# Kernel optimization log

Measured on AMD Instinct MI355X. Metric: run time of the kernel, lower is better.

Reference implementation:

```python
import jax, jax.numpy as jnp
import numpy as np

INV_SCALE_SQ = 0.25  # module __init__ arg
N_SITES = 65536
SITE_DIM = 5  # (x, y, r, g, b)
H, W = 2048, 2048


def setup_inputs() -> dict:
    key = jax.random.key(0)
    k1, k2, k3, k4 = jax.random.split(key, 4)
    # site positions uniform over the image, colors uniform in [0,1]
    pos = jax.random.uniform(k1, (N_SITES, 2), dtype=jnp.float32) * jnp.array([W, H], jnp.float32)
    col = jax.random.uniform(k2, (N_SITES, 3), dtype=jnp.float32)
    sites = jnp.concatenate([pos, col], axis=-1)  # [N,5]
    cand0 = jax.random.randint(k3, (H, W), 0, N_SITES, dtype=jnp.int32)
    cand1 = jax.random.randint(k4, (H, W), 0, N_SITES, dtype=jnp.int32)
    return {"sites": sites, "cand0": cand0, "cand1": cand1, "width": W, "height": H}


def reference(sites, cand0, cand1, width, height):
    # per-pixel soft (anti-aliased) Voronoi rasterization of colored sites
    xs = jnp.arange(width, dtype=jnp.float32) + 0.5
    ys = jnp.arange(height, dtype=jnp.float32) + 0.5
    px = jnp.stack(jnp.meshgrid(xs, ys, indexing="xy"), axis=-1)  # [H,W,2] pixel centers
    s0 = sites[cand0]  # [H,W,5] gather candidate 0
    s1 = sites[cand1]  # [H,W,5] gather candidate 1
    d0 = jnp.sum((px - s0[..., :2]) ** 2, axis=-1)  # squared dist to site0
    d1 = jnp.sum((px - s1[..., :2]) ** 2, axis=-1)
    w = jax.nn.sigmoid((d1 - d0) * INV_SCALE_SQ)[..., None]  # weight toward closer site0
    out = w * s0[..., 2:] + (1.0 - w) * s1[..., 2:]  # [H,W,3]
    return out
```

## Files before the change

### kernel.cpp

```cpp
#include <hip/hip_runtime.h>
#include <hip/hip_fp16.h>


#define IMG_W 2048
#define IMG_H 2048
#define N_PIX (IMG_W * IMG_H)
#define N_SITES 65536
#define INV_SCALE_SQ 0.25f

typedef int   vint4   __attribute__((ext_vector_type(4)));
typedef float vfloat4 __attribute__((ext_vector_type(4)));

__global__ __launch_bounds__(256) void repack_sites(
    const float* __restrict__ sites, vfloat4* __restrict__ packed)
{
    const int i = blockIdx.x * blockDim.x + threadIdx.x;
    const float* s = sites + (size_t)i * 5;
    const __half2 rg = __floats2half2_rn(s[2], s[3]);
    const __half2 b0 = __floats2half2_rn(s[4], 0.0f);
    vfloat4 v;
    v.x = s[0];
    v.y = s[1];
    v.z = __uint_as_float(*reinterpret_cast<const unsigned int*>(&rg));
    v.w = __uint_as_float(*reinterpret_cast<const unsigned int*>(&b0));
    packed[i] = v;
}

__device__ __forceinline__ float3 unpack_rgb(const vfloat4& rec) {
    const unsigned int zu = __float_as_uint(rec.z);
    const unsigned int wu = __float_as_uint(rec.w);
    const __half2 rg = *reinterpret_cast<const __half2*>(&zu);
    const __half2 b0 = *reinterpret_cast<const __half2*>(&wu);
    const float2 rgf = __half22float2(rg);
    return make_float3(rgf.x, rgf.y, __half2float(b0.x));
}

__global__ __launch_bounds__(256) void voronoi_soft_kernel(
    const vfloat4* __restrict__ packed,
    const int*     __restrict__ cand0,
    const int*     __restrict__ cand1,
    float*         __restrict__ out)
{
    const int tid = blockIdx.x * blockDim.x + threadIdx.x;
    const int pix = tid * 4;

    const vint4 c0 = __builtin_nontemporal_load(reinterpret_cast<const vint4*>(cand0 + pix));
    const vint4 c1 = __builtin_nontemporal_load(reinterpret_cast<const vint4*>(cand1 + pix));
    const int idx0[4] = {c0.x, c0.y, c0.z, c0.w};
    const int idx1[4] = {c1.x, c1.y, c1.z, c1.w};

    vfloat4 r0[4], r1[4];
#pragma unroll
    for (int i = 0; i < 4; ++i) r0[i] = packed[idx0[i]];
#pragma unroll
    for (int i = 0; i < 4; ++i) r1[i] = packed[idx1[i]];

    const float py = (float)(pix >> 11) + 0.5f;
    const float px_base = (float)(pix & (IMG_W - 1)) + 0.5f;

    float res[12];
#pragma unroll
    for (int i = 0; i < 4; ++i) {
        const float px = px_base + (float)i;
        const float dx0 = px - r0[i].x, dy0 = py - r0[i].y;
        const float dx1 = px - r1[i].x, dy1 = py - r1[i].y;
        const float d0 = dx0 * dx0 + dy0 * dy0;
        const float d1 = dx1 * dx1 + dy1 * dy1;

        const float t = (d1 - d0) * INV_SCALE_SQ;
        const float w = 1.0f / (1.0f + __expf(-t));
        const float wc = 1.0f - w;

        const float3 cA = unpack_rgb(r0[i]);
        const float3 cB = unpack_rgb(r1[i]);
        res[i * 3 + 0] = w * cA.x + wc * cB.x;
        res[i * 3 + 1] = w * cA.y + wc * cB.y;
        res[i * 3 + 2] = w * cA.z + wc * cB.z;
    }

    vfloat4* o = reinterpret_cast<vfloat4*>(out + (size_t)pix * 3);
    vfloat4 o0 = {res[0], res[1], res[2], res[3]};
    vfloat4 o1 = {res[4], res[5], res[6], res[7]};
    vfloat4 o2 = {res[8], res[9], res[10], res[11]};
    o[0] = o0;
    o[1] = o1;
    o[2] = o2;
}

__global__ __launch_bounds__(256) void voronoi_soft_fallback(
    const float* __restrict__ sites,
    const int*   __restrict__ cand0,
    const int*   __restrict__ cand1,
    float*       __restrict__ out)
{
    const int tid = blockIdx.x * blockDim.x + threadIdx.x;
    const int pix = tid * 4;
    const int4 c0 = *reinterpret_cast<const int4*>(cand0 + pix);
    const int4 c1 = *reinterpret_cast<const int4*>(cand1 + pix);
    const int idx0[4] = {c0.x, c0.y, c0.z, c0.w};
    const int idx1[4] = {c1.x, c1.y, c1.z, c1.w};
    const float py = (float)(pix >> 11) + 0.5f;
    const float px_base = (float)(pix & (IMG_W - 1)) + 0.5f;
    float res[12];
#pragma unroll
    for (int i = 0; i < 4; ++i) {
        const float px = px_base + (float)i;
        const float* s0 = sites + (size_t)idx0[i] * 5;
        const float* s1 = sites + (size_t)idx1[i] * 5;
        const float dx0 = px - s0[0], dy0 = py - s0[1];
        const float dx1 = px - s1[0], dy1 = py - s1[1];
        const float d0 = dx0 * dx0 + dy0 * dy0;
        const float d1 = dx1 * dx1 + dy1 * dy1;
        const float w = 1.0f / (1.0f + __expf(-(d1 - d0) * INV_SCALE_SQ));
        const float wc = 1.0f - w;
        res[i * 3 + 0] = w * s0[2] + wc * s1[2];
        res[i * 3 + 1] = w * s0[3] + wc * s1[3];
        res[i * 3 + 2] = w * s0[4] + wc * s1[4];
    }
    float4* o = reinterpret_cast<float4*>(out + (size_t)pix * 3);
    o[0] = make_float4(res[0], res[1], res[2], res[3]);
    o[1] = make_float4(res[4], res[5], res[6], res[7]);
    o[2] = make_float4(res[8], res[9], res[10], res[11]);
}

extern "C" void kernel_launch(void* const* d_in, const int* in_sizes, int n_in,
                              void* d_out, int out_size, void* d_ws, size_t ws_size,
                              hipStream_t stream) {
    const float* sites = (const float*)d_in[0];
    const int*   cand0 = (const int*)d_in[1];
    const int*   cand1 = (const int*)d_in[2];
    float* out = (float*)d_out;

    const int threads = 256;
    const int blocks = N_PIX / (4 * threads);

    const size_t packed_bytes = (size_t)N_SITES * sizeof(vfloat4);
    if (ws_size >= packed_bytes) {
        vfloat4* packed = (vfloat4*)d_ws;
        repack_sites<<<N_SITES / 256, 256, 0, stream>>>(sites, packed);
        voronoi_soft_kernel<<<blocks, threads, 0, stream>>>(packed, cand0, cand1, out);
    } else {
        voronoi_soft_fallback<<<blocks, threads, 0, stream>>>(sites, cand0, cand1, out);
    }
}
```

Measured before the change: 136.2 us.

## Process eight pixels per thread with inline-asm gathers and staged waitcnt

Each thread now handles eight pixels instead of four, issuing all sixteen site gathers up front through inline global_load_dwordx4 assembly with the sc0 cache bit. A partial s_waitcnt lets the first four pixels be shaded while the second batch of loads is still in flight. The goal is more memory-level parallelism per thread to hide gather latency. In exchange, register pressure rises, the grid has half as many threads, and hand-written waitcnt code bypasses compiler scheduling and depends on it counting outstanding loads correctly.

```diff
diff --git a/kernel.cpp b/kernel.cpp
--- a/kernel.cpp
+++ b/kernel.cpp
@@ -35,6 +35,28 @@
     return make_float3(rgf.x, rgf.y, __half2float(b0.x));
 }
 
+__device__ __forceinline__ void shade4(
+    const vfloat4* r0, const vfloat4* r1,
+    float px_base, float py, float* res )
+{
+#pragma unroll
+    for (int i = 0; i < 4; ++i) {
+        const float px = px_base + (float)i;
+        const float dx0 = px - r0[i].x, dy0 = py - r0[i].y;
+        const float dx1 = px - r1[i].x, dy1 = py - r1[i].y;
+        const float d0 = dx0 * dx0 + dy0 * dy0;
+        const float d1 = dx1 * dx1 + dy1 * dy1;
+        const float t = (d1 - d0) * INV_SCALE_SQ;
+        const float w = 1.0f / (1.0f + __expf(-t));
+        const float wc = 1.0f - w;
+        const float3 cA = unpack_rgb(r0[i]);
+        const float3 cB = unpack_rgb(r1[i]);
+        res[i * 3 + 0] = w * cA.x + wc * cB.x;
+        res[i * 3 + 1] = w * cA.y + wc * cB.y;
+        res[i * 3 + 2] = w * cA.z + wc * cB.z;
+    }
+}
+
 __global__ __launch_bounds__(256) void voronoi_soft_kernel(
     const vfloat4* __restrict__ packed,
     const int*     __restrict__ cand0,
@@ -42,49 +64,77 @@
     float*         __restrict__ out)
 {
     const int tid = blockIdx.x * blockDim.x + threadIdx.x;
-    const int pix = tid * 4;
+    const int pix = tid * 8;
 
-    const vint4 c0 = __builtin_nontemporal_load(reinterpret_cast<const vint4*>(cand0 + pix));
-    const vint4 c1 = __builtin_nontemporal_load(reinterpret_cast<const vint4*>(cand1 + pix));
-    const int idx0[4] = {c0.x, c0.y, c0.z, c0.w};
-    const int idx1[4] = {c1.x, c1.y, c1.z, c1.w};
+    const vint4* c0p = reinterpret_cast<const vint4*>(cand0 + pix);
+    const vint4* c1p = reinterpret_cast<const vint4*>(cand1 + pix);
+    const vint4 c0lo = __builtin_nontemporal_load(c0p);
+    const vint4 c0hi = __builtin_nontemporal_load(c0p + 1);
+    const vint4 c1lo = __builtin_nontemporal_load(c1p);
+    const vint4 c1hi = __builtin_nontemporal_load(c1p + 1);
 
-    vfloat4 r0[4], r1[4];
-#pragma unroll
-    for (int i = 0; i < 4; ++i) r0[i] = packed[idx0[i]];
-#pragma unroll
-    for (int i = 0; i < 4; ++i) r1[i] = packed[idx1[i]];
+    const int oa0[4] = {c0lo.x << 4, c0lo.y << 4, c0lo.z << 4, c0lo.w << 4};
+    const int oa1[4] = {c1lo.x << 4, c1lo.y << 4, c1lo.z << 4, c1lo.w << 4};
+    const int ob0[4] = {c0hi.x << 4, c0hi.y << 4, c0hi.z << 4, c0hi.w << 4};
+    const int ob1[4] = {c1hi.x << 4, c1hi.y << 4, c1hi.z << 4, c1hi.w << 4};
+
+    vfloat4 a0[4], a1[4];
+    vfloat4 b0[4], b1[4];
+
+    asm volatile(
+        "global_load_dwordx4 %0, %8, %16 sc0\n\t"
+        "global_load_dwordx4 %1, %9, %16 sc0\n\t"
+        "global_load_dwordx4 %2, %10, %16 sc0\n\t"
+        "global_load_dwordx4 %3, %11, %16 sc0\n\t"
+        "global_load_dwordx4 %4, %12, %16 sc0\n\t"
+        "global_load_dwordx4 %5, %13, %16 sc0\n\t"
+        "global_load_dwordx4 %6, %14, %16 sc0\n\t"
+        "global_load_dwordx4 %7, %15, %16 sc0"
+        : "=&v"(a0[0]), "=&v"(a0[1]), "=&v"(a0[2]), "=&v"(a0[3]),
+          "=&v"(a1[0]), "=&v"(a1[1]), "=&v"(a1[2]), "=&v"(a1[3])
+        : "v"(oa0[0]), "v"(oa0[1]), "v"(oa0[2]), "v"(oa0[3]),
+          "v"(oa1[0]), "v"(oa1[1]), "v"(oa1[2]), "v"(oa1[3]),
+          "s"(packed)
+        : "memory");
+
+    asm volatile(
+        "global_load_dwordx4 %0, %16, %24 sc0\n\t"
+        "global_load_dwordx4 %1, %17, %24 sc0\n\t"
+        "global_load_dwordx4 %2, %18, %24 sc0\n\t"
+        "global_load_dwordx4 %3, %19, %24 sc0\n\t"
+        "global_load_dwordx4 %4, %20, %24 sc0\n\t"
+        "global_load_dwordx4 %5, %21, %24 sc0\n\t"
+        "global_load_dwordx4 %6, %22, %24 sc0\n\t"
+        "global_load_dwordx4 %7, %23, %24 sc0\n\t"
+        "s_waitcnt vmcnt(8)"
+        : "=&v"(b0[0]), "=&v"(b0[1]), "=&v"(b0[2]), "=&v"(b0[3]),
+          "=&v"(b1[0]), "=&v"(b1[1]), "=&v"(b1[2]), "=&v"(b1[3]),
+          "+v"(a0[0]), "+v"(a0[1]), "+v"(a0[2]), "+v"(a0[3]),
+          "+v"(a1[0]), "+v"(a1[1]), "+v"(a1[2]), "+v"(a1[3])
+        : "v"(ob0[0]), "v"(ob0[1]), "v"(ob0[2]), "v"(ob0[3]),
+          "v"(ob1[0]), "v"(ob1[1]), "v"(ob1[2]), "v"(ob1[3]),
+          "s"(packed)
+        : "memory");
 
     const float py = (float)(pix >> 11) + 0.5f;
     const float px_base = (float)(pix & (IMG_W - 1)) + 0.5f;
 
-    float res[12];
-#pragma unroll
-    for (int i = 0; i < 4; ++i) {
-        const float px = px_base + (float)i;
-        const float dx0 = px - r0[i].x, dy0 = py - r0[i].y;
-        const float dx1 = px - r1[i].x, dy1 = py - r1[i].y;
-        const float d0 = dx0 * dx0 + dy0 * dy0;
-        const float d1 = dx1 * dx1 + dy1 * dy1;
+    float res[24];
+    shade4(a0, a1, px_base, py, res);
 
-        const float t = (d1 - d0) * INV_SCALE_SQ;
-        const float w = 1.0f / (1.0f + __expf(-t));
-        const float wc = 1.0f - w;
+    asm volatile(
+        "s_waitcnt vmcnt(0)"
+        : "+v"(b0[0]), "+v"(b0[1]), "+v"(b0[2]), "+v"(b0[3]),
+          "+v"(b1[0]), "+v"(b1[1]), "+v"(b1[2]), "+v"(b1[3]));
 
-        const float3 cA = unpack_rgb(r0[i]);
-        const float3 cB = unpack_rgb(r1[i]);
-        res[i * 3 + 0] = w * cA.x + wc * cB.x;
-        res[i * 3 + 1] = w * cA.y + wc * cB.y;
-        res[i * 3 + 2] = w * cA.z + wc * cB.z;
-    }
+    shade4(b0, b1, px_base + 4.0f, py, res + 12);
 
     vfloat4* o = reinterpret_cast<vfloat4*>(out + (size_t)pix * 3);
-    vfloat4 o0 = {res[0], res[1], res[2], res[3]};
-    vfloat4 o1 = {res[4], res[5], res[6], res[7]};
-    vfloat4 o2 = {res[8], res[9], res[10], res[11]};
-    o[0] = o0;
-    o[1] = o1;
-    o[2] = o2;
+#pragma unroll
+    for (int k = 0; k < 6; ++k) {
+        vfloat4 v = {res[k * 4 + 0], res[k * 4 + 1], res[k * 4 + 2], res[k * 4 + 3]};
+        o[k] = v;
+    }
 }
 
 __global__ __launch_bounds__(256) void voronoi_soft_fallback(
@@ -131,15 +181,13 @@
     const int*   cand1 = (const int*)d_in[2];
     float* out = (float*)d_out;
 
-    const int threads = 256;
-    const int blocks = N_PIX / (4 * threads);
-
     const size_t packed_bytes = (size_t)N_SITES * sizeof(vfloat4);
     if (ws_size >= packed_bytes) {
         vfloat4* packed = (vfloat4*)d_ws;
         repack_sites<<<N_SITES / 256, 256, 0, stream>>>(sites, packed);
-        voronoi_soft_kernel<<<blocks, threads, 0, stream>>>(packed, cand0, cand1, out);
+        const int blocks = N_PIX / (8 * 256);
+        voronoi_soft_kernel<<<blocks, 256, 0, stream>>>(packed, cand0, cand1, out);
     } else {
-        voronoi_soft_fallback<<<blocks, threads, 0, stream>>>(sites, cand0, cand1, out);
+        voronoi_soft_fallback<<<N_PIX / (4 * 256), 256, 0, stream>>>(sites, cand0, cand1, out);
     }
 }
```

New measurement: 137.0 us. About the same (+0.6%).

## Process one pixel per thread with inline-asm sc0 gathers of packed sites

Applied to the files above, without the earlier changes.

Changes the main kernel from four pixels per thread to one pixel per thread, launching four times as many blocks. Each thread does scalar candidate loads and issues the two site gathers through inline global_load_dwordx4 with the sc0 cache-policy bit, followed by an explicit wait. The aim is more memory-level parallelism through many more waves and different cache handling for the random gathers. The cost is scalar 4-byte loads and stores in place of 16-byte vector accesses, and an asm waitcnt that blocks the compiler from scheduling around the loads.

```diff
diff --git a/kernel.cpp b/kernel.cpp
--- a/kernel.cpp
+++ b/kernel.cpp
@@ -8,7 +8,6 @@
 #define N_SITES 65536
 #define INV_SCALE_SQ 0.25f
 
-typedef int   vint4   __attribute__((ext_vector_type(4)));
 typedef float vfloat4 __attribute__((ext_vector_type(4)));
 
 __global__ __launch_bounds__(256) void repack_sites(
@@ -41,50 +40,41 @@
     const int*     __restrict__ cand1,
     float*         __restrict__ out)
 {
-    const int tid = blockIdx.x * blockDim.x + threadIdx.x;
-    const int pix = tid * 4;
+    const int pix = blockIdx.x * blockDim.x + threadIdx.x;
 
-    const vint4 c0 = __builtin_nontemporal_load(reinterpret_cast<const vint4*>(cand0 + pix));
-    const vint4 c1 = __builtin_nontemporal_load(reinterpret_cast<const vint4*>(cand1 + pix));
-    const int idx0[4] = {c0.x, c0.y, c0.z, c0.w};
-    const int idx1[4] = {c1.x, c1.y, c1.z, c1.w};
+    const int i0 = __builtin_nontemporal_load(cand0 + pix);
+    const int i1 = __builtin_nontemporal_load(cand1 + pix);
 
-    vfloat4 r0[4], r1[4];
-#pragma unroll
-    for (int i = 0; i < 4; ++i) r0[i] = packed[idx0[i]];
-#pragma unroll
-    for (int i = 0; i < 4; ++i) r1[i] = packed[idx1[i]];
+    const int o0 = i0 << 4;
+    const int o1 = i1 << 4;
+
+    vfloat4 r0, r1;
+    asm volatile(
+        "global_load_dwordx4 %0, %2, %4 sc0\n\t"
+        "global_load_dwordx4 %1, %3, %4 sc0\n\t"
+        "s_waitcnt vmcnt(0)"
+        : "=&v"(r0), "=&v"(r1)
+        : "v"(o0), "v"(o1), "s"(packed)
+        : "memory");
 
     const float py = (float)(pix >> 11) + 0.5f;
-    const float px_base = (float)(pix & (IMG_W - 1)) + 0.5f;
+    const float px = (float)(pix & (IMG_W - 1)) + 0.5f;
 
-    float res[12];
-#pragma unroll
-    for (int i = 0; i < 4; ++i) {
-        const float px = px_base + (float)i;
-        const float dx0 = px - r0[i].x, dy0 = py - r0[i].y;
-        const float dx1 = px - r1[i].x, dy1 = py - r1[i].y;
-        const float d0 = dx0 * dx0 + dy0 * dy0;
-        const float d1 = dx1 * dx1 + dy1 * dy1;
+    const float dx0 = px - r0.x, dy0 = py - r0.y;
+    const float dx1 = px - r1.x, dy1 = py - r1.y;
+    const float d0 = dx0 * dx0 + dy0 * dy0;
+    const float d1 = dx1 * dx1 + dy1 * dy1;
+    const float t = (d1 - d0) * INV_SCALE_SQ;
+    const float w = 1.0f / (1.0f + __expf(-t));
+    const float wc = 1.0f - w;
 
-        const float t = (d1 - d0) * INV_SCALE_SQ;
-        const float w = 1.0f / (1.0f + __expf(-t));
-        const float wc = 1.0f - w;
+    const float3 cA = unpack_rgb(r0);
+    const float3 cB = unpack_rgb(r1);
 
-        const float3 cA = unpack_rgb(r0[i]);
-        const float3 cB = unpack_rgb(r1[i]);
-        res[i * 3 + 0] = w * cA.x + wc * cB.x;
-        res[i * 3 + 1] = w * cA.y + wc * cB.y;
-        res[i * 3 + 2] = w * cA.z + wc * cB.z;
-    }
-
-    vfloat4* o = reinterpret_cast<vfloat4*>(out + (size_t)pix * 3);
-    vfloat4 o0 = {res[0], res[1], res[2], res[3]};
-    vfloat4 o1 = {res[4], res[5], res[6], res[7]};
-    vfloat4 o2 = {res[8], res[9], res[10], res[11]};
-    o[0] = o0;
-    o[1] = o1;
-    o[2] = o2;
+    float* o = out + (size_t)pix * 3;
+    o[0] = w * cA.x + wc * cB.x;
+    o[1] = w * cA.y + wc * cB.y;
+    o[2] = w * cA.z + wc * cB.z;
 }
 
 __global__ __launch_bounds__(256) void voronoi_soft_fallback(
@@ -131,15 +121,12 @@
     const int*   cand1 = (const int*)d_in[2];
     float* out = (float*)d_out;
 
-    const int threads = 256;
-    const int blocks = N_PIX / (4 * threads);
-
     const size_t packed_bytes = (size_t)N_SITES * sizeof(vfloat4);
     if (ws_size >= packed_bytes) {
         vfloat4* packed = (vfloat4*)d_ws;
         repack_sites<<<N_SITES / 256, 256, 0, stream>>>(sites, packed);
-        voronoi_soft_kernel<<<blocks, threads, 0, stream>>>(packed, cand0, cand1, out);
+        voronoi_soft_kernel<<<N_PIX / 256, 256, 0, stream>>>(packed, cand0, cand1, out);
     } else {
-        voronoi_soft_fallback<<<blocks, threads, 0, stream>>>(sites, cand0, cand1, out);
+        voronoi_soft_fallback<<<N_PIX / (4 * 256), 256, 0, stream>>>(sites, cand0, cand1, out);
     }
 }
```

New measurement: 130.3 us. 1.05x faster.
